# Optimization experiments

Hardware: AMD Instinct MI355X
Metric: run time of the kernel (lower is better)

## Reference

```python
import jax, jax.numpy as jnp
import numpy as np

B, N, C = 8, 1024, 768
H = 12
HD = C // H  # 64


def setup_inputs() -> dict:
    key = jax.random.key(0)
    k1, k2, k3, k4 = jax.random.split(key, 4)
    x = jax.random.normal(k1, (B, N, C), dtype=jnp.float32)
    # nn.Linear(dim, 3*dim, bias=False): weight shape [3C, C]
    w_qkv = jax.random.normal(k2, (3 * C, C), dtype=jnp.float32) * (C ** -0.5)
    # nn.Linear(dim, dim): weight [C, C], bias [C]
    w_proj = jax.random.normal(k3, (C, C), dtype=jnp.float32) * (C ** -0.5)
    b_proj = jax.random.normal(k4, (C,), dtype=jnp.float32) * 0.01
    return {"x": x, "w_qkv": w_qkv, "w_proj": w_proj, "b_proj": b_proj}


def reference(x, w_qkv, w_proj, b_proj):
    scale = HD ** -0.5
    qkv = jnp.einsum("bnc,dc->bnd", x, w_qkv)  # [B,N,3C]
    qkv = qkv.reshape(B, N, 3, H, HD).transpose(2, 0, 3, 1, 4)  # [3,B,H,N,HD]
    q, k, v = qkv[0], qkv[1], qkv[2]
    attn = jnp.einsum("bhqd,bhkd->bhqk", q, k) * scale  # [B,H,N,N]
    attn = jax.nn.softmax(attn, axis=-1)
    out = jnp.einsum("bhqk,bhkd->bhqd", attn, v)  # [B,H,N,HD]
    out = out.transpose(0, 2, 1, 3).reshape(B, N, C)
    return jnp.einsum("bnc,dc->bnd", out, w_proj) + b_proj
```

## Files before the change

### kernel.cpp

```cpp
#include <hip/hip_runtime.h>
#include <hip/hip_bf16.h>


typedef __attribute__((ext_vector_type(8))) short bf16x8;
typedef __attribute__((ext_vector_type(4))) float f32x4;
typedef __attribute__((ext_vector_type(4))) short s16x4;

static constexpr int BB  = 8;
static constexpr int SEQ = 1024;
static constexpr int CH  = 768;
static constexpr int NH  = 12;
static constexpr int HD  = 64;
static constexpr int MT  = BB * SEQ;
static constexpr int C3  = 3 * CH;

__device__ __forceinline__ float bf2f(short s) {
    unsigned u = ((unsigned)(unsigned short)s) << 16;
    return __builtin_bit_cast(float, u);
}
__device__ __forceinline__ short f2bf(float f) {
    unsigned u = __builtin_bit_cast(unsigned, f);
    u += 0x7FFF + ((u >> 16) & 1);
    return (short)(u >> 16);
}
__device__ __forceinline__ unsigned pack_bf2(float lo, float hi) {
    unsigned ul = __builtin_bit_cast(unsigned, lo) + 0x8000u;
    unsigned uh = __builtin_bit_cast(unsigned, hi) + 0x8000u;
    return __builtin_amdgcn_perm(uh, ul, 0x07060302);
}
__device__ __forceinline__ void async16(const short* g, short* l) {
    __builtin_amdgcn_global_load_lds(
        (const __attribute__((address_space(1))) void*)g,
        (__attribute__((address_space(3))) void*)l, 16, 0, 0);
}

__global__ __launch_bounds__(256) void cvt3(
    const float* __restrict__ a, short* __restrict__ da, int na,
    const float* __restrict__ b, short* __restrict__ db, int nb,
    const float* __restrict__ c, short* __restrict__ dc, int nc)
{
    long i = (long)(blockIdx.x * 256 + threadIdx.x) * 8;
    const float* s; short* d; long off;
    if (i < na)                 { s = a; d = da; off = i; }
    else if (i < (long)na + nb) { s = b; d = db; off = i - na; }
    else                        { s = c; d = dc; off = i - na - nb; }
    float4 x0 = *(const float4*)&s[off];
    float4 x1 = *(const float4*)&s[off + 4];
    bf16x8 o;
    o[0] = f2bf(x0.x); o[1] = f2bf(x0.y); o[2] = f2bf(x0.z); o[3] = f2bf(x0.w);
    o[4] = f2bf(x1.x); o[5] = f2bf(x1.y); o[6] = f2bf(x1.z); o[7] = f2bf(x1.w);
    *(bf16x8*)&d[off] = o;
}

template <bool F32OUT>
__global__ __launch_bounds__(256, 4) void gemm_bt(
    const short* __restrict__ A, const short* __restrict__ Bt,
    const float* __restrict__ bias, void* __restrict__ outp,
    int Ndim, int K)
{
    __shared__ __align__(16) short As[128 * 64];
    __shared__ __align__(16) short Bs[128 * 64];
    const int tid  = threadIdx.x;
    const int wave = tid >> 6, lane = tid & 63;
    const int quad = lane >> 4, l16 = lane & 15;
    const int wr = wave >> 1, wc = wave & 1;
    const int row0 = blockIdx.y * 128, col0 = blockIdx.x * 128;

    f32x4 acc[4][4] = {};

    for (int kb = 0; kb < K; kb += 64) {
        #pragma unroll
        for (int p = 0; p < 4; ++p) {
            int g = p * 256 + wave * 64 + lane;
            int r = g >> 3, cb = (g & 7) * 8;
            async16(&A[(long)(row0 + r) * K + kb + cb], &As[(p * 256 + wave * 64) * 8]);
            async16(&Bt[(long)(col0 + r) * K + kb + cb], &Bs[(p * 256 + wave * 64) * 8]);
        }
        __syncthreads();

        #pragma unroll
        for (int kh = 0; kh < 2; ++kh) {
            bf16x8 af[4], bfr[4];
            #pragma unroll
            for (int mi = 0; mi < 4; ++mi)
                af[mi] = *(const bf16x8*)&As[(wr * 64 + mi * 16 + l16) * 64 + kh * 32 + quad * 8];
            #pragma unroll
            for (int ni = 0; ni < 4; ++ni)
                bfr[ni] = *(const bf16x8*)&Bs[(wc * 64 + ni * 16 + l16) * 64 + kh * 32 + quad * 8];
            #pragma unroll
            for (int mi = 0; mi < 4; ++mi)
                #pragma unroll
                for (int ni = 0; ni < 4; ++ni)
                    acc[mi][ni] = __builtin_amdgcn_mfma_f32_16x16x32_bf16(
                        af[mi], bfr[ni], acc[mi][ni], 0, 0, 0);
        }
        __syncthreads();
    }

    #pragma unroll
    for (int mi = 0; mi < 4; ++mi) {
        #pragma unroll
        for (int ni = 0; ni < 4; ++ni) {
            int col = col0 + wc * 64 + ni * 16 + l16;
            float bv = bias ? bias[col] : 0.0f;
            #pragma unroll
            for (int r = 0; r < 4; ++r) {
                int row = row0 + wr * 64 + mi * 16 + quad * 4 + r;
                if (F32OUT)
                    ((float*)outp)[(long)row * Ndim + col] = acc[mi][ni][r] + bv;
                else
                    ((short*)outp)[(long)row * Ndim + col] = f2bf(acc[mi][ni][r] + bv);
            }
        }
    }
}

__global__ __launch_bounds__(256, 3) void attn(
    const short* __restrict__ qkv, short* __restrict__ attout)
{
    constexpr int STK = 72, STV = 68, STP = 68;
    __shared__ __align__(16) short Ks [2][64 * STK];
    __shared__ __align__(16) short Vts[2][64 * STV];
    __shared__ __align__(16) short Ps [4][16 * STP];
    const int tid  = threadIdx.x;
    const int wave = tid >> 6, lane = tid & 63;
    const int quad = lane >> 4, l16 = lane & 15;
    const int hb = blockIdx.x, h = hb % NH, b = hb / NH;
    const int qbase = blockIdx.y * 128;
    const long base = (long)b * SEQ * C3;

    bf16x8 aq[2][2];
    #pragma unroll
    for (int qt = 0; qt < 2; ++qt) {
        const long qp = base + (long)(qbase + qt * 64 + wave * 16 + l16) * C3 + h * HD;
        aq[qt][0] = *(const bf16x8*)&qkv[qp + quad * 8];
        aq[qt][1] = *(const bf16x8*)&qkv[qp + 32 + quad * 8];
        #pragma unroll
        for (int j = 0; j < 8; ++j) {
            aq[qt][0][j] = f2bf(bf2f(aq[qt][0][j]) * 0.125f);
            aq[qt][1][j] = f2bf(bf2f(aq[qt][1][j]) * 0.125f);
        }
    }

    bf16x8 onesv;
    #pragma unroll
    for (int j = 0; j < 8; ++j) onesv[j] = (short)0x3F80;

    f32x4 acc[2][4] = {};
    f32x4 accl[2] = {};

    const int kr = tid >> 3, kc = (tid & 7) * 8;
    const short* kp0 = qkv + base + (long)kr * C3 + (CH + h * HD) + kc;
    const short* kp1 = kp0 + (long)32 * C3;
    const short* vp  = qkv + base + (long)lane * C3 + (2 * CH + h * HD) + wave * 16;

    bf16x8 k0r, k1r, v0r, v1r;
    k0r = *(const bf16x8*)kp0;
    k1r = *(const bf16x8*)kp1;
    v0r = *(const bf16x8*)vp;
    v1r = *(const bf16x8*)(vp + 8);

    const int nit = SEQ / 64;
    for (int it = 0; it < nit; ++it) {
        const int bufi = it & 1;
        *(bf16x8*)&Ks[bufi][kr * STK + kc]        = k0r;
        *(bf16x8*)&Ks[bufi][(kr + 32) * STK + kc] = k1r;
        #pragma unroll
        for (int j = 0; j < 8; ++j) {
            Vts[bufi][(wave * 16 + j) * STV + lane]     = v0r[j];
            Vts[bufi][(wave * 16 + 8 + j) * STV + lane] = v1r[j];
        }
        if (it + 1 < nit) {
            kp0 += (long)64 * C3; kp1 += (long)64 * C3; vp += (long)64 * C3;
            k0r = *(const bf16x8*)kp0;
            k1r = *(const bf16x8*)kp1;
            v0r = *(const bf16x8*)vp;
            v1r = *(const bf16x8*)(vp + 8);
        }
        __syncthreads();
        const short* Kb = Ks[bufi];
        const short* Vb = Vts[bufi];

        #pragma unroll
        for (int qt = 0; qt < 2; ++qt) {
            f32x4 St[4];
            #pragma unroll
            for (int t = 0; t < 4; ++t) {
                bf16x8 k0 = *(const bf16x8*)&Kb[(t * 16 + l16) * STK + quad * 8];
                bf16x8 k1 = *(const bf16x8*)&Kb[(t * 16 + l16) * STK + 32 + quad * 8];
                f32x4 s = {};
                s = __builtin_amdgcn_mfma_f32_16x16x32_bf16(k0, aq[qt][0], s, 0, 0, 0);
                s = __builtin_amdgcn_mfma_f32_16x16x32_bf16(k1, aq[qt][1], s, 0, 0, 0);
                St[t] = s;
            }

            #pragma unroll
            for (int t = 0; t < 4; ++t) {
                unsigned w0 = pack_bf2(__expf(St[t][0]), __expf(St[t][1]));
                unsigned w1 = pack_bf2(__expf(St[t][2]), __expf(St[t][3]));
                uint2 pk; pk.x = w0; pk.y = w1;
                *(uint2*)&Ps[wave][l16 * STP + t * 16 + quad * 4] = pk;
            }

            #pragma unroll
            for (int kt = 0; kt < 2; ++kt) {
                bf16x8 pf;
                *(s16x4*)&pf         = *(const s16x4*)&Ps[wave][l16 * STP + kt * 32 + quad * 8];
                *(((s16x4*)&pf) + 1) = *(const s16x4*)&Ps[wave][l16 * STP + kt * 32 + quad * 8 + 4];
                accl[qt] = __builtin_amdgcn_mfma_f32_16x16x32_bf16(pf, onesv, accl[qt], 0, 0, 0);
                #pragma unroll
                for (int nb = 0; nb < 4; ++nb) {
                    bf16x8 vf;
                    *(s16x4*)&vf         = *(const s16x4*)&Vb[(nb * 16 + l16) * STV + kt * 32 + quad * 8];
                    *(((s16x4*)&vf) + 1) = *(const s16x4*)&Vb[(nb * 16 + l16) * STV + kt * 32 + quad * 8 + 4];
                    acc[qt][nb] = __builtin_amdgcn_mfma_f32_16x16x32_bf16(pf, vf, acc[qt][nb], 0, 0, 0);
                }
            }
        }
    }

    #pragma unroll
    for (int qt = 0; qt < 2; ++qt) {
        #pragma unroll
        for (int r = 0; r < 4; ++r) {
            float linv = 1.0f / accl[qt][r];
            int row = qbase + qt * 64 + wave * 16 + quad * 4 + r;
            #pragma unroll
            for (int nb = 0; nb < 4; ++nb)
                attout[((long)b * SEQ + row) * CH + h * HD + nb * 16 + l16] =
                    f2bf(acc[qt][nb][r] * linv);
        }
    }
}

extern "C" void kernel_launch(void* const* d_in, const int* in_sizes, int n_in,
                              void* d_out, int out_size, void* d_ws, size_t ws_size,
                              hipStream_t stream) {
    const float* x      = (const float*)d_in[0];
    const float* w_qkv  = (const float*)d_in[1];
    const float* w_proj = (const float*)d_in[2];
    const float* b_proj = (const float*)d_in[3];

    const int nx = MT * CH, nq = C3 * CH, np = CH * CH;

    short* xb      = (short*)d_ws;
    short* wqkvb   = xb + nx;
    short* wprojb  = wqkvb + nq;
    short* qkv     = wprojb + np;
    short* attnout = xb;

    cvt3<<<(nx + nq + np) / 2048, 256, 0, stream>>>(
        x, xb, nx, w_qkv, wqkvb, nq, w_proj, wprojb, np);

    gemm_bt<false><<<dim3(C3 / 128, MT / 128), 256, 0, stream>>>(
        xb, wqkvb, nullptr, qkv, C3, CH);
    attn<<<dim3(96, 8), 256, 0, stream>>>(qkv, attnout);
    gemm_bt<true><<<dim3(CH / 128, MT / 128), 256, 0, stream>>>(
        attnout, wprojb, b_proj, (float*)d_out, CH, CH);
}
```

Measured before the change: 207.6 us.

## Keep softmax probabilities in registers and permute V layout to match MFMA operand

```diff
diff --git a/kernel.cpp b/kernel.cpp
--- a/kernel.cpp
+++ b/kernel.cpp
@@ -118,10 +118,9 @@
 __global__ __launch_bounds__(256, 3) void attn(
     const short* __restrict__ qkv, short* __restrict__ attout)
 {
-    constexpr int STK = 72, STV = 68, STP = 68;
+    constexpr int STK = 72, STV = 68;
     __shared__ __align__(16) short Ks [2][64 * STK];
     __shared__ __align__(16) short Vts[2][64 * STV];
-    __shared__ __align__(16) short Ps [4][16 * STP];
     const int tid  = threadIdx.x;
     const int wave = tid >> 6, lane = tid & 63;
     const int quad = lane >> 4, l16 = lane & 15;
@@ -150,9 +149,10 @@
     f32x4 accl[2] = {};
 
     const int kr = tid >> 3, kc = (tid & 7) * 8;
+    const int vr = tid >> 2, vc = (tid & 3) * 16;
     const short* kp0 = qkv + base + (long)kr * C3 + (CH + h * HD) + kc;
     const short* kp1 = kp0 + (long)32 * C3;
-    const short* vp  = qkv + base + (long)lane * C3 + (2 * CH + h * HD) + wave * 16;
+    const short* vp  = qkv + base + (long)vr * C3 + (2 * CH + h * HD) + vc;
 
     bf16x8 k0r, k1r, v0r, v1r;
     k0r = *(const bf16x8*)kp0;
@@ -167,8 +167,8 @@
         *(bf16x8*)&Ks[bufi][(kr + 32) * STK + kc] = k1r;
         #pragma unroll
         for (int j = 0; j < 8; ++j) {
-            Vts[bufi][(wave * 16 + j) * STV + lane]     = v0r[j];
-            Vts[bufi][(wave * 16 + 8 + j) * STV + lane] = v1r[j];
+            Vts[bufi][(vc + j) * STV + vr]     = v0r[j];
+            Vts[bufi][(vc + 8 + j) * STV + vr] = v1r[j];
         }
         if (it + 1 < nit) {
             kp0 += (long)64 * C3; kp1 += (long)64 * C3; vp += (long)64 * C3;
@@ -194,25 +194,27 @@
                 St[t] = s;
             }
 
-            #pragma unroll
-            for (int t = 0; t < 4; ++t) {
-                unsigned w0 = pack_bf2(__expf(St[t][0]), __expf(St[t][1]));
-                unsigned w1 = pack_bf2(__expf(St[t][2]), __expf(St[t][3]));
-                uint2 pk; pk.x = w0; pk.y = w1;
-                *(uint2*)&Ps[wave][l16 * STP + t * 16 + quad * 4] = pk;
-            }
+            float p[4][4];
+            #pragma unroll
+            for (int t = 0; t < 4; ++t)
+                #pragma unroll
+                for (int r = 0; r < 4; ++r) p[t][r] = __expf(St[t][r]);
 
             #pragma unroll
             for (int kt = 0; kt < 2; ++kt) {
                 bf16x8 pf;
-                *(s16x4*)&pf         = *(const s16x4*)&Ps[wave][l16 * STP + kt * 32 + quad * 8];
-                *(((s16x4*)&pf) + 1) = *(const s16x4*)&Ps[wave][l16 * STP + kt * 32 + quad * 8 + 4];
+                unsigned* pw = (unsigned*)&pf;
+                pw[0] = pack_bf2(p[2 * kt][0],     p[2 * kt][1]);
+                pw[1] = pack_bf2(p[2 * kt][2],     p[2 * kt][3]);
+                pw[2] = pack_bf2(p[2 * kt + 1][0], p[2 * kt + 1][1]);
+                pw[3] = pack_bf2(p[2 * kt + 1][2], p[2 * kt + 1][3]);
                 accl[qt] = __builtin_amdgcn_mfma_f32_16x16x32_bf16(pf, onesv, accl[qt], 0, 0, 0);
                 #pragma unroll
                 for (int nb = 0; nb < 4; ++nb) {
+                    const short* vrow = &Vb[(nb * 16 + l16) * STV + kt * 32 + quad * 4];
                     bf16x8 vf;
-                    *(s16x4*)&vf         = *(const s16x4*)&Vb[(nb * 16 + l16) * STV + kt * 32 + quad * 8];
-                    *(((s16x4*)&vf) + 1) = *(const s16x4*)&Vb[(nb * 16 + l16) * STV + kt * 32 + quad * 8 + 4];
+                    *(s16x4*)&vf         = *(const s16x4*)vrow;
+                    *(((s16x4*)&vf) + 1) = *(const s16x4*)(vrow + 16);
                     acc[qt][nb] = __builtin_amdgcn_mfma_f32_16x16x32_bf16(pf, vf, acc[qt][nb], 0, 0, 0);
                 }
             }
```

Result: faster. 193.8 us (-6.6%).
